# Performance work log

Measured on AMD Instinct MI355X. Metric: run time of the kernel, lower is better.

The kernel has to match this reference:

```python
import jax, jax.numpy as jnp
import numpy as np

H = 4        # nhead
TEMP = 0.1   # temperature
TOP_K = 5
SHAPE_EPS = 1e-5


def _ln(x, g, b):
    m = x.mean(-1, keepdims=True)
    v = ((x - m) ** 2).mean(-1, keepdims=True)
    return (x - m) / jnp.sqrt(v + SHAPE_EPS) * g + b


def _mha(x, Wqkv, bqkv, Wo, bo):
    B, L, D = x.shape
    Dh = D // H
    qkv = x @ Wqkv.T + bqkv                     # [B,L,3D]
    q, k, v = jnp.split(qkv, 3, axis=-1)
    q = q.reshape(B, L, H, Dh)
    k = k.reshape(B, L, H, Dh)
    v = v.reshape(B, L, H, Dh)
    att = jnp.einsum('bqhd,bkhd->bhqk', q, k) * (1.0 / np.sqrt(Dh))
    att = jax.nn.softmax(att, axis=-1)
    o = jnp.einsum('bhqk,bkhd->bqhd', att, v).reshape(B, L, D)
    return o @ Wo.T + bo


def _pattern_encoder(x, cls_token, Wqkv, bqkv, Wo, bo, ln1_g, ln1_b,
                     W1, b1, W2, b2, ln2_g, ln2_b, proj_W, proj_b, proj_g, proj_bb):
    B, L, D = x.shape
    h = jnp.concatenate([jnp.broadcast_to(cls_token, (B, 1, D)), x], axis=1)  # [B,L+1,D]
    for i in range(Wqkv.shape[0]):  # num_layers=2, post-norm (PyTorch default)
        a = _mha(h, Wqkv[i], bqkv[i], Wo[i], bo[i])
        h = _ln(h + a, ln1_g[i], ln1_b[i])
        f = jax.nn.gelu(h @ W1[i].T + b1[i], approximate=False) @ W2[i].T + b2[i]
        h = _ln(h + f, ln2_g[i], ln2_b[i])
    cls_out = h[:, 0, :]
    return _ln(cls_out @ proj_W.T + proj_b, proj_g, proj_bb)  # [B,d_repr]


def _value_encoder(xm, vW1, vb1, v_g, v_b, vW2, vb2):
    hh = _ln(xm @ vW1.T + vb1, v_g, v_b)
    return jax.nn.gelu(hh, approximate=False) @ vW2.T + vb2


def setup_inputs() -> dict:
    B, L, D, DR, N, P, NL = 64, 512, 512, 128, 10000, 96, 2
    key = jax.random.key(0)
    ks = jax.random.split(key, 16)
    sc = 0.02
    inp = {
        'query': jax.random.normal(ks[0], (B, L, D), jnp.float32),
        'memory_keys': jax.random.normal(ks[1], (N, DR), jnp.float32),
        'memory_values': jax.random.normal(ks[2], (N, P, D), jnp.float32),
        'cls_token': jax.random.normal(ks[3], (1, 1, D), jnp.float32) * sc,
        'Wqkv': jax.random.normal(ks[4], (NL, 3 * D, D), jnp.float32) * sc,
        'bqkv': jnp.zeros((NL, 3 * D), jnp.float32),
        'Wo': jax.random.normal(ks[5], (NL, D, D), jnp.float32) * sc,
        'bo': jnp.zeros((NL, D), jnp.float32),
        'ln1_g': jnp.ones((NL, D), jnp.float32),
        'ln1_b': jnp.zeros((NL, D), jnp.float32),
        'W1': jax.random.normal(ks[6], (NL, 2 * D, D), jnp.float32) * sc,
        'b1': jnp.zeros((NL, 2 * D), jnp.float32),
        'W2': jax.random.normal(ks[7], (NL, D, 2 * D), jnp.float32) * sc,
        'b2': jnp.zeros((NL, D), jnp.float32),
        'ln2_g': jnp.ones((NL, D), jnp.float32),
        'ln2_b': jnp.zeros((NL, D), jnp.float32),
        'proj_W': jax.random.normal(ks[8], (DR, D), jnp.float32) * sc,
        'proj_b': jnp.zeros((DR,), jnp.float32),
        'proj_g': jnp.ones((DR,), jnp.float32),
        'proj_bb': jnp.zeros((DR,), jnp.float32),
        'vW1': jax.random.normal(ks[9], (DR, D), jnp.float32) * sc,
        'vb1': jnp.zeros((DR,), jnp.float32),
        'v_g': jnp.ones((DR,), jnp.float32),
        'v_b': jnp.zeros((DR,), jnp.float32),
        'vW2': jax.random.normal(ks[10], (DR, DR), jnp.float32) * sc,
        'vb2': jnp.zeros((DR,), jnp.float32),
        'shape_w': jnp.float32(0.5),
    }
    return inp


def reference(query, memory_keys, memory_values, cls_token, Wqkv, bqkv, Wo, bo,
              ln1_g, ln1_b, W1, b1, W2, b2, ln2_g, ln2_b,
              proj_W, proj_b, proj_g, proj_bb, vW1, vb1, v_g, v_b, vW2, vb2, shape_w):
    q_repr = _pattern_encoder(query, cls_token, Wqkv, bqkv, Wo, bo, ln1_g, ln1_b,
                              W1, b1, W2, b2, ln2_g, ln2_b, proj_W, proj_b, proj_g, proj_bb)
    q_val = _value_encoder(query.mean(axis=1), vW1, vb1, v_g, v_b, vW2, vb2)
    qk = shape_w * q_repr + (1.0 - shape_w) * q_val              # [B,DR]
    # squared euclidean distance, expanded form (same math as sum((a-b)^2))
    d = ((qk ** 2).sum(-1)[:, None]
         - 2.0 * qk @ memory_keys.T
         + (memory_keys ** 2).sum(-1)[None, :])                  # [B,N]
    sim = -d / TEMP
    top_scores, top_idx = jax.lax.top_k(sim, TOP_K)              # [B,K]
    weights = jax.nn.softmax(top_scores, axis=-1)
    retrieved = memory_values[top_idx]                           # [B,K,P,D]
    return retrieved, weights
```

## Files before the change

kernel.cpp:

```cpp
#include <hip/hip_runtime.h>
#include <math.h>

#define B_    64
#define LQ    512
#define LC    513
#define DD    512
#define HH    4
#define DH    128
#define DRr   128
#define NKEYS 10000
#define PP    96
#define TOPK  5
#define MROWS (B_*LC)
#define VTSTRIDE 544

typedef __attribute__((ext_vector_type(8))) short short8v;
typedef __attribute__((ext_vector_type(4))) float f32x4;
typedef __attribute__((ext_vector_type(16))) float f32x16;

static __device__ __forceinline__ float gelu_exact(float x) {
    return 0.5f * x * (1.0f + erff(x * 0.70710678118654752440f));
}

static __device__ __forceinline__ unsigned short f2bf(float x) {
    union { float f; unsigned u; } v; v.f = x;
    unsigned r = v.u + 0x7fff + ((v.u >> 16) & 1);
    return (unsigned short)(r >> 16);
}
static __device__ __forceinline__ float bf2f(unsigned short h) {
    union { float f; unsigned u; } v; v.u = ((unsigned)h) << 16;
    return v.f;
}
static __device__ __forceinline__ void split_bf(float x, unsigned short& hi, unsigned short& lo) {
    hi = f2bf(x);
    lo = f2bf(x - bf2f(hi));
}

static __device__ __forceinline__ int xcd_swz(int orig, int nwg) {
    int xcd = orig & 7;
    int lid = orig >> 3;
    int q = nwg >> 3, r = nwg & 7;
    int base = (xcd < r) ? xcd * (q + 1) : r * (q + 1) + (xcd - r) * q;
    return base + lid;
}

static __device__ __forceinline__ void gload16(const unsigned short* g, unsigned short* l) {
    __builtin_amdgcn_global_load_lds(
        (const __attribute__((address_space(1))) unsigned*)g,
        (__attribute__((address_space(3))) unsigned*)l, 16, 0, 0);
}

__global__ __launch_bounds__(256)
void split_kernel(const float* __restrict__ x, unsigned short* __restrict__ hi,
                  unsigned short* __restrict__ lo, int n4)
{
    int i = blockIdx.x * blockDim.x + threadIdx.x;
    if (i >= n4) return;
    float4 v = ((const float4*)x)[i];
    unsigned short h0,h1,h2,h3,l0,l1,l2,l3;
    split_bf(v.x,h0,l0); split_bf(v.y,h1,l1); split_bf(v.z,h2,l2); split_bf(v.w,h3,l3);
    ((uint2*)hi)[i] = make_uint2((unsigned)h0 | ((unsigned)h1 << 16), (unsigned)h2 | ((unsigned)h3 << 16));
    ((uint2*)lo)[i] = make_uint2((unsigned)l0 | ((unsigned)l1 << 16), (unsigned)l2 | ((unsigned)l3 << 16));
}

__global__ __launch_bounds__(128)
void concat_cls(const float* __restrict__ query, const float* __restrict__ cls,
                float* __restrict__ h, unsigned short* __restrict__ h_hi,
                unsigned short* __restrict__ h_lo)
{
    int row = blockIdx.x;
    int t = threadIdx.x;
    int b = row / LC, r = row - b * LC;
    const float* src = (r == 0) ? cls : (query + ((size_t)b * LQ + (r - 1)) * DD);
    float4 v = *(const float4*)(src + t * 4);
    *(float4*)(h + (size_t)row * DD + t * 4) = v;
    unsigned short hs[4], ls[4];
    split_bf(v.x, hs[0], ls[0]); split_bf(v.y, hs[1], ls[1]);
    split_bf(v.z, hs[2], ls[2]); split_bf(v.w, hs[3], ls[3]);
    size_t o = (size_t)row * DD + t * 4;
    ((uint2*)(h_hi))[o >> 2] = make_uint2((unsigned)hs[0] | ((unsigned)hs[1]<<16),
                                          (unsigned)hs[2] | ((unsigned)hs[3]<<16));
    ((uint2*)(h_lo))[o >> 2] = make_uint2((unsigned)ls[0] | ((unsigned)ls[1]<<16),
                                          (unsigned)ls[2] | ((unsigned)ls[3]<<16));
}

#define BM 128
#define BN 128
#define BK 32

#define MFMA32(a, b, c) __builtin_amdgcn_mfma_f32_32x32x16_bf16(a, b, c, 0, 0, 0)

template<int MODE>
__global__ __launch_bounds__(256)
void gemm3(const unsigned short* __restrict__ Ahi, const unsigned short* __restrict__ Alo,
           const unsigned short* __restrict__ Whi, const unsigned short* __restrict__ Wlo,
           const float* __restrict__ bias, const float* __restrict__ res,
           float* __restrict__ Cf, unsigned short* __restrict__ Chi,
           unsigned short* __restrict__ Clo, unsigned* __restrict__ Vix,
           int M, int N, int K, int NBN)
{
    __shared__ __align__(16) unsigned short POOL[16384];
    unsigned short* LAh = POOL;
    unsigned short* LAl = POOL + 4096;
    unsigned short* LBh = POOL + 8192;
    unsigned short* LBl = POOL + 12288;

    const int t = threadIdx.x;
    const int lane = t & 63, w = t >> 6;
    const int wr = w >> 1, wc = w & 1;
    const int wg = xcd_swz(blockIdx.x, gridDim.x);
    const int bm = wg / NBN, bn = wg - bm * NBN;
    const int row0 = bm * BM, col0 = bn * BN;

    const int srow = t >> 2;
    const int sg   = t & 3;
    const int glog = sg ^ (srow & 3);
    int ar0 = row0 + srow;      if (ar0 >= M) ar0 = M - 1;
    int ar1 = row0 + srow + 64; if (ar1 >= M) ar1 = M - 1;
    const size_t aoff0 = (size_t)ar0 * K + glog * 8;
    const size_t aoff1 = (size_t)ar1 * K + glog * 8;
    const size_t boff0 = (size_t)(col0 + srow) * K + glog * 8;
    const size_t boff1 = (size_t)(col0 + srow + 64) * K + glog * 8;
    const int ldso0 = t * 8;
    const int ldso1 = t * 8 + 2048;

    f32x16 acc[2][2];
    #pragma unroll
    for (int m = 0; m < 2; m++)
        #pragma unroll
        for (int n = 0; n < 2; n++)
            #pragma unroll
            for (int i = 0; i < 16; i++) acc[m][n][i] = 0.f;

    const int cl = lane & 31;
    const int kg = lane >> 5;
    const int cl3 = cl & 3;

    const int KT = K / BK;
    for (int kt = 0; kt < KT; kt++) {
        const int k0 = kt * BK;
        __syncthreads();
        gload16(Ahi + aoff0 + k0, &LAh[ldso0]);
        gload16(Ahi + aoff1 + k0, &LAh[ldso1]);
        gload16(Alo + aoff0 + k0, &LAl[ldso0]);
        gload16(Alo + aoff1 + k0, &LAl[ldso1]);
        gload16(Whi + boff0 + k0, &LBh[ldso0]);
        gload16(Whi + boff1 + k0, &LBh[ldso1]);
        gload16(Wlo + boff0 + k0, &LBl[ldso0]);
        gload16(Wlo + boff1 + k0, &LBl[ldso1]);
        __syncthreads();

        #pragma unroll
        for (int ks = 0; ks < 2; ks++) {
            const int blkswz = ((ks * 2 + kg) ^ cl3) * 8;
            short8v ah[2], al[2], bh[2], bl[2];
            #pragma unroll
            for (int m = 0; m < 2; m++) {
                int off = (wr * 64 + m * 32 + cl) * 32 + blkswz;
                ah[m] = *(const short8v*)&LAh[off];
                al[m] = *(const short8v*)&LAl[off];
            }
            #pragma unroll
            for (int n = 0; n < 2; n++) {
                int off = (wc * 64 + n * 32 + cl) * 32 + blkswz;
                bh[n] = *(const short8v*)&LBh[off];
                bl[n] = *(const short8v*)&LBl[off];
            }
            #pragma unroll
            for (int m = 0; m < 2; m++)
                #pragma unroll
                for (int n = 0; n < 2; n++) {
                    acc[m][n] = MFMA32(ah[m], bh[n], acc[m][n]);
                    acc[m][n] = MFMA32(al[m], bh[n], acc[m][n]);
                    acc[m][n] = MFMA32(ah[m], bl[n], acc[m][n]);
                }
        }
    }

    if (MODE == 3 && col0 >= 1024) {
        const int hh = (col0 - 1024) >> 7;
        unsigned* VS = (unsigned*)POOL;
        const int bb0 = row0 / LC;
        const int bound = (bb0 + 1) * LC;
        const int ddl = t >> 3, j0 = (t & 7) * 16;
        #pragma unroll
        for (int p = 0; p < 4; p++) {
            __syncthreads();
            if (wc == (p >> 1)) {
                const int ccl = col0 + wc * 64 + (p & 1) * 32 + cl;
                const float bcol = bias[ccl];
                #pragma unroll
                for (int m = 0; m < 2; m++) {
                    const int lrb = wr * 64 + m * 32 + 4 * kg;
                    #pragma unroll
                    for (int q = 0; q < 4; q++)
                        #pragma unroll
                        for (int r = 0; r < 4; r++) {
                            float v = ((p & 1) ? acc[m][1][q * 4 + r]
                                               : acc[m][0][q * 4 + r]) + bcol;
                            unsigned short hv, lv;
                            split_bf(v, hv, lv);
                            VS[cl * 129 + lrb + 8 * q + r] =
                                (unsigned)hv | ((unsigned)lv << 16);
                        }
                }
            }
            __syncthreads();
            long long vb0 = (long long)((bb0 * HH + hh) * DH + p * 32 + ddl) * VTSTRIDE
                            - (long long)bb0 * LC;
            long long vb1 = (long long)(((bb0 + 1) * HH + hh) * DH + p * 32 + ddl) * VTSTRIDE
                            - (long long)(bb0 + 1) * LC;
            #pragma unroll
            for (int j = 0; j < 16; j++) {
                int row = row0 + j0 + j;
                if (row < M) {
                    long long vi = (row < bound ? vb0 : vb1) + row;
                    Vix[vi] = VS[ddl * 129 + j0 + j];
                }
            }
        }
        return;
    }

    #pragma unroll
    for (int m = 0; m < 2; m++) {
        const int rb = row0 + wr * 64 + m * 32 + 4 * kg;
        #pragma unroll
        for (int n = 0; n < 2; n++) {
            const int cc = col0 + wc * 64 + n * 32 + cl;
            const float bcol = bias[cc];
            #pragma unroll
            for (int q = 0; q < 4; q++) {
                #pragma unroll
                for (int r = 0; r < 4; r++) {
                    int row = rb + 8 * q + r;
                    if (row < M) {
                        float v = acc[m][n][q * 4 + r] + bcol;
                        if (MODE == 1) v += res[(size_t)row * N + cc];
                        if (MODE == 2) {
                            v = gelu_exact(v);
                            unsigned short hv, lv;
                            split_bf(v, hv, lv);
                            Chi[(size_t)row * N + cc] = hv;
                            Clo[(size_t)row * N + cc] = lv;
                        } else if (MODE == 3) {
                            unsigned short hv, lv;
                            split_bf(v, hv, lv);
                            Chi[(size_t)row * 1024 + cc] = hv;
                            Clo[(size_t)row * 1024 + cc] = lv;
                        } else {
                            Cf[(size_t)row * N + cc] = v;
                        }
                    }
                }
            }
        }
    }
}

#define AQT 64
#define AKT 32
#define NKT2 17
#define MFMA16(a, b, c) __builtin_amdgcn_mfma_f32_16x16x32_bf16(a, b, c, 0, 0, 0)
__global__ __launch_bounds__(256)
void attn_mfma(const unsigned short* __restrict__ qkhi, const unsigned short* __restrict__ qklo,
               const unsigned* __restrict__ vtx,
               unsigned short* __restrict__ ohi, unsigned short* __restrict__ olo)
{
    __shared__ __align__(16) unsigned short SM[24064];
    #define KH(r,d) SM[(r)*136 + (d)]
    #define KL(r,d) SM[4352 + (r)*136 + (d)]
    #define VH(d,k) SM[8704 + (d)*40 + (k)]
    #define VL(d,k) SM[13824 + (d)*40 + (k)]
    #define PH(r,k) SM[18944 + (r)*40 + (k)]
    #define PL(r,k) SM[21504 + (r)*40 + (k)]
    #define OS(r,d) SM[(r)*136 + (d)]

    const int t = threadIdx.x;
    const int lane = t & 63, w = t >> 6;
    const int id = xcd_swz(blockIdx.x, gridDim.x);
    const int qt = id % 9;
    const int hb = id / 9;
    const int h = hb & 3, b = hb >> 2;
    const int q0 = qt * AQT;
    const int c = lane & 15, g = lane >> 4;
    const float SCALE = 0.08838834764831845f;

    short8v qh[4], ql[4];
    {
        int qrow = b * LC + q0 + w * 16 + c;
        if (qrow > MROWS - 1) qrow = MROWS - 1;
        const unsigned short* bh_ = qkhi + (size_t)qrow * 1024 + h * DH;
        const unsigned short* bl_ = qklo + (size_t)qrow * 1024 + h * DH;
        #pragma unroll
        for (int ks = 0; ks < 4; ks++) {
            qh[ks] = *(const short8v*)(bh_ + ks * 32 + g * 8);
            ql[ks] = *(const short8v*)(bl_ + ks * 32 + g * 8);
        }
    }

    float m_r[4], l_r[4];
    #pragma unroll
    for (int r = 0; r < 4; r++) { m_r[r] = -INFINITY; l_r[r] = 0.f; }
    f32x4 acc_o[8];
    #pragma unroll
    for (int n = 0; n < 8; n++) { acc_o[n][0]=0.f; acc_o[n][1]=0.f; acc_o[n][2]=0.f; acc_o[n][3]=0.f; }

    const int skr = t >> 3, skd = (t & 7) * 16;
    const int svd = t >> 1, svk = (t & 1) * 16;

    for (int kt = 0; kt < NKT2; kt++) {
        __syncthreads();
        {
            int krow = b * LC + kt * AKT + skr;
            if (krow > MROWS - 1) krow = MROWS - 1;
            const unsigned short* kb  = qkhi + (size_t)krow * 1024 + 512 + h * DH + skd;
            const unsigned short* kbl = qklo + (size_t)krow * 1024 + 512 + h * DH + skd;
            *(short8v*)&KH(skr, skd)     = *(const short8v*)kb;
            *(short8v*)&KH(skr, skd + 8) = *(const short8v*)(kb + 8);
            *(short8v*)&KL(skr, skd)     = *(const short8v*)kbl;
            *(short8v*)&KL(skr, skd + 8) = *(const short8v*)(kbl + 8);
            const unsigned* vb = vtx + ((size_t)((b * HH + h) * DH + svd)) * VTSTRIDE + kt * AKT + svk;
            uint4 a0 = *(const uint4*)(vb);
            uint4 a1 = *(const uint4*)(vb + 4);
            uint4 a2 = *(const uint4*)(vb + 8);
            uint4 a3 = *(const uint4*)(vb + 12);
            uint4 hA, hB, lA, lB;
            hA.x = (a0.x & 0xffffu) | (a0.y << 16);
            hA.y = (a0.z & 0xffffu) | (a0.w << 16);
            hA.z = (a1.x & 0xffffu) | (a1.y << 16);
            hA.w = (a1.z & 0xffffu) | (a1.w << 16);
            hB.x = (a2.x & 0xffffu) | (a2.y << 16);
            hB.y = (a2.z & 0xffffu) | (a2.w << 16);
            hB.z = (a3.x & 0xffffu) | (a3.y << 16);
            hB.w = (a3.z & 0xffffu) | (a3.w << 16);
            lA.x = (a0.x >> 16) | (a0.y & 0xffff0000u);
            lA.y = (a0.z >> 16) | (a0.w & 0xffff0000u);
            lA.z = (a1.x >> 16) | (a1.y & 0xffff0000u);
            lA.w = (a1.z >> 16) | (a1.w & 0xffff0000u);
            lB.x = (a2.x >> 16) | (a2.y & 0xffff0000u);
            lB.y = (a2.z >> 16) | (a2.w & 0xffff0000u);
            lB.z = (a3.x >> 16) | (a3.y & 0xffff0000u);
            lB.w = (a3.z >> 16) | (a3.w & 0xffff0000u);
            *(uint4*)&VH(svd, svk)     = hA;
            *(uint4*)&VH(svd, svk + 8) = hB;
            *(uint4*)&VL(svd, svk)     = lA;
            *(uint4*)&VL(svd, svk + 8) = lB;
        }
        __syncthreads();

        f32x4 s[2];
        s[0][0]=s[0][1]=s[0][2]=s[0][3]=0.f;
        s[1][0]=s[1][1]=s[1][2]=s[1][3]=0.f;
        #pragma unroll
        for (int n = 0; n < 2; n++) {
            #pragma unroll
            for (int ks = 0; ks < 4; ks++) {
                short8v kh = *(const short8v*)&KH(n * 16 + c, ks * 32 + g * 8);
                short8v kl = *(const short8v*)&KL(n * 16 + c, ks * 32 + g * 8);
                s[n] = MFMA16(qh[ks], kh, s[n]);
                s[n] = MFMA16(ql[ks], kh, s[n]);
                s[n] = MFMA16(qh[ks], kl, s[n]);
            }
        }

        #pragma unroll
        for (int n = 0; n < 2; n++) {
            bool oob = (kt * 32 + n * 16 + c) >= LC;
            #pragma unroll
            for (int r = 0; r < 4; r++) {
                float sv = s[n][r] * SCALE;
                s[n][r] = oob ? -INFINITY : sv;
            }
        }

        float alpha[4], p0v[4], p1v[4];
        #pragma unroll
        for (int r = 0; r < 4; r++) {
            float rm = fmaxf(s[0][r], s[1][r]);
            #pragma unroll
            for (int off = 1; off < 16; off <<= 1) rm = fmaxf(rm, __shfl_xor(rm, off));
            float mn = fmaxf(m_r[r], rm);
            float p0 = expf(s[0][r] - mn);
            float p1 = expf(s[1][r] - mn);
            float ts = p0 + p1;
            #pragma unroll
            for (int off = 1; off < 16; off <<= 1) ts += __shfl_xor(ts, off);
            float al = expf(m_r[r] - mn);
            m_r[r] = mn;
            l_r[r] = al * l_r[r] + ts;
            alpha[r] = al;
            p0v[r] = p0; p1v[r] = p1;
        }

        #pragma unroll
        for (int n = 0; n < 8; n++)
            #pragma unroll
            for (int r = 0; r < 4; r++) acc_o[n][r] *= alpha[r];

        #pragma unroll
        for (int r = 0; r < 4; r++) {
            unsigned short ph, pl;
            split_bf(p0v[r], ph, pl);
            PH(w * 16 + g * 4 + r, c) = ph;
            PL(w * 16 + g * 4 + r, c) = pl;
            split_bf(p1v[r], ph, pl);
            PH(w * 16 + g * 4 + r, 16 + c) = ph;
            PL(w * 16 + g * 4 + r, 16 + c) = pl;
        }
        __syncthreads();

        short8v pah = *(const short8v*)&PH(w * 16 + c, g * 8);
        short8v pal = *(const short8v*)&PL(w * 16 + c, g * 8);
        #pragma unroll
        for (int n = 0; n < 8; n++) {
            short8v vh = *(const short8v*)&VH(n * 16 + c, g * 8);
            short8v vl = *(const short8v*)&VL(n * 16 + c, g * 8);
            acc_o[n] = MFMA16(pah, vh, acc_o[n]);
            acc_o[n] = MFMA16(pal, vh, acc_o[n]);
            acc_o[n] = MFMA16(pah, vl, acc_o[n]);
        }
    }

    float inv[4];
    #pragma unroll
    for (int r = 0; r < 4; r++) inv[r] = 1.0f / l_r[r];

    const int orow = t >> 2, oc0 = (t & 3) * 32;
    #pragma unroll
    for (int pass = 0; pass < 2; pass++) {
        __syncthreads();
        #pragma unroll
        for (int n = 0; n < 8; n++)
            #pragma unroll
            for (int r = 0; r < 4; r++) {
                float v = acc_o[n][r] * inv[r];
                unsigned short hv, lv;
                split_bf(v, hv, lv);
                OS(w * 16 + g * 4 + r, n * 16 + c) = pass ? lv : hv;
            }
        __syncthreads();
        int grow = q0 + orow;
        if (grow < LC) {
            unsigned short* dst = (pass ? olo : ohi) + ((size_t)(b * LC + grow)) * DD + h * DH + oc0;
            #pragma unroll
            for (int u = 0; u < 4; u++)
                *(short8v*)(dst + u * 8) = *(const short8v*)&OS(orow, oc0 + u * 8);
        }
    }
    #undef KH
    #undef KL
    #undef VH
    #undef VL
    #undef PH
    #undef PL
    #undef OS
}

__global__ __launch_bounds__(128)
void ln512(const float* __restrict__ X, const float* __restrict__ g,
           const float* __restrict__ bb, float* __restrict__ Y,
           unsigned short* __restrict__ Yhi, unsigned short* __restrict__ Ylo)
{
    __shared__ float red[2];
    int row = blockIdx.x, t = threadIdx.x;
    const float* x = X + (size_t)row * DD;
    float4 v = *(const float4*)(x + t * 4);
    float s = v.x + v.y + v.z + v.w;
    #pragma unroll
    for (int off = 1; off < 64; off <<= 1) s += __shfl_xor(s, off);
    if ((t & 63) == 0) red[t >> 6] = s;
    __syncthreads();
    float mean = (red[0] + red[1]) * (1.0f / 512.0f);
    __syncthreads();
    float d0 = v.x - mean, d1 = v.y - mean, d2 = v.z - mean, d3 = v.w - mean;
    float s2 = d0 * d0 + d1 * d1 + d2 * d2 + d3 * d3;
    #pragma unroll
    for (int off = 1; off < 64; off <<= 1) s2 += __shfl_xor(s2, off);
    if ((t & 63) == 0) red[t >> 6] = s2;
    __syncthreads();
    float var = (red[0] + red[1]) * (1.0f / 512.0f);
    float rstd = 1.0f / sqrtf(var + 1e-5f);
    float4 gv = *(const float4*)(g + t * 4);
    float4 bv = *(const float4*)(bb + t * 4);
    float4 ov;
    ov.x = d0 * rstd * gv.x + bv.x;
    ov.y = d1 * rstd * gv.y + bv.y;
    ov.z = d2 * rstd * gv.z + bv.z;
    ov.w = d3 * rstd * gv.w + bv.w;
    size_t o = (size_t)row * DD + t * 4;
    *(float4*)(Y + o) = ov;
    unsigned short hs[4], ls[4];
    split_bf(ov.x, hs[0], ls[0]); split_bf(ov.y, hs[1], ls[1]);
    split_bf(ov.z, hs[2], ls[2]); split_bf(ov.w, hs[3], ls[3]);
    ((uint2*)Yhi)[o >> 2] = make_uint2((unsigned)hs[0] | ((unsigned)hs[1]<<16),
                                       (unsigned)hs[2] | ((unsigned)hs[3]<<16));
    ((uint2*)Ylo)[o >> 2] = make_uint2((unsigned)ls[0] | ((unsigned)ls[1]<<16),
                                       (unsigned)ls[2] | ((unsigned)ls[3]<<16));
}

__global__ __launch_bounds__(128)
void mean_part(const float* __restrict__ query, float* __restrict__ part)
{
    int b = blockIdx.x, ch = blockIdx.y, t = threadIdx.x;
    const float* base = query + ((size_t)b * LQ + ch * 64) * DD + t * 4;
    float ax = 0.f, ay = 0.f, az = 0.f, aw = 0.f;
    for (int l = 0; l < 64; l++) {
        float4 v = *(const float4*)(base + (size_t)l * DD);
        ax += v.x; ay += v.y; az += v.z; aw += v.w;
    }
    *(float4*)(part + ((size_t)(b * 8 + ch)) * DD + t * 4) = make_float4(ax, ay, az, aw);
}

__global__ __launch_bounds__(128)
void mean_fin(const float* __restrict__ part, float* __restrict__ xm)
{
    int b = blockIdx.x, t = threadIdx.x;
    float ax = 0.f, ay = 0.f, az = 0.f, aw = 0.f;
    #pragma unroll
    for (int ch = 0; ch < 8; ch++) {
        float4 v = *(const float4*)(part + ((size_t)(b * 8 + ch)) * DD + t * 4);
        ax += v.x; ay += v.y; az += v.z; aw += v.w;
    }
    *(float4*)(xm + (size_t)b * DD + t * 4) =
        make_float4(ax * (1.f/512.f), ay * (1.f/512.f), az * (1.f/512.f), aw * (1.f/512.f));
}

static __device__ __forceinline__ float block128_sum(float x, float* red, int t) {
    #pragma unroll
    for (int off = 1; off < 64; off <<= 1) x += __shfl_xor(x, off);
    if ((t & 63) == 0) red[t >> 6] = x;
    __syncthreads();
    float r = red[0] + red[1];
    __syncthreads();
    return r;
}

__global__ __launch_bounds__(128)
void proj_ln(const float* __restrict__ h, const float* __restrict__ pW, const float* __restrict__ pb,
             const float* __restrict__ pg, const float* __restrict__ pbb, float* __restrict__ q_repr)
{
    __shared__ float xs[DD];
    __shared__ float red[2];
    int b = blockIdx.x, t = threadIdx.x;
    *(float4*)&xs[t * 4] = *(const float4*)(h + (size_t)(b * LC) * DD + t * 4);
    __syncthreads();
    const float* w = pW + (size_t)t * DD;
    float acc = pb[t];
    for (int k = 0; k < DD; k += 4) {
        float4 a = *(const float4*)&xs[k];
        float4 ww = *(const float4*)(w + k);
        acc += a.x * ww.x + a.y * ww.y + a.z * ww.z + a.w * ww.w;
    }
    float mean = block128_sum(acc, red, t) * (1.f / 128.f);
    float dx = acc - mean;
    float var = block128_sum(dx * dx, red, t) * (1.f / 128.f);
    float rstd = 1.0f / sqrtf(var + 1e-5f);
    q_repr[(size_t)b * DRr + t] = dx * rstd * pg[t] + pbb[t];
}

__global__ __launch_bounds__(128)
void venc(const float* __restrict__ xm, const float* __restrict__ vW1, const float* __restrict__ vb1,
          const float* __restrict__ vg, const float* __restrict__ vb,
          const float* __restrict__ vW2, const float* __restrict__ vb2,
          float* __restrict__ q_val)
{
    __shared__ float xs[DD];
    __shared__ float hg[DRr];
    __shared__ float red[2];
    int b = blockIdx.x, t = threadIdx.x;
    *(float4*)&xs[t * 4] = *(const float4*)(xm + (size_t)b * DD + t * 4);
    __syncthreads();
    const float* w = vW1 + (size_t)t * DD;
    float acc = vb1[t];
    for (int k = 0; k < DD; k += 4) {
        float4 a = *(const float4*)&xs[k];
        float4 ww = *(const float4*)(w + k);
        acc += a.x * ww.x + a.y * ww.y + a.z * ww.z + a.w * ww.w;
    }
    float mean = block128_sum(acc, red, t) * (1.f / 128.f);
    float dx = acc - mean;
    float var = block128_sum(dx * dx, red, t) * (1.f / 128.f);
    float rstd = 1.0f / sqrtf(var + 1e-5f);
    float hn = dx * rstd * vg[t] + vb[t];
    hg[t] = gelu_exact(hn);
    __syncthreads();
    const float* w2 = vW2 + (size_t)t * DRr;
    float acc2 = vb2[t];
    for (int k = 0; k < DRr; k += 4) {
        float4 a = *(const float4*)&hg[k];
        float4 ww = *(const float4*)(w2 + k);
        acc2 += a.x * ww.x + a.y * ww.y + a.z * ww.z + a.w * ww.w;
    }
    q_val[(size_t)b * DRr + t] = acc2;
}

__global__ void combine_qk(const float* __restrict__ qr, const float* __restrict__ qv,
                           const float* __restrict__ swp, float* __restrict__ qk)
{
    int i = blockIdx.x * blockDim.x + threadIdx.x;
    if (i < B_ * DRr) {
        float sw = swp[0];
        qk[i] = sw * qr[i] + (1.f - sw) * qv[i];
    }
}

#define SIMCH 10
__global__ __launch_bounds__(256)
void sim_kernel(const float* __restrict__ qk, const float* __restrict__ mkeys, float* __restrict__ sim)
{
    __shared__ float qs[DRr];
    int b = blockIdx.x, ch = blockIdx.y, t = threadIdx.x;
    if (t < DRr) qs[t] = qk[(size_t)b * DRr + t];
    __syncthreads();
    float qn = 0.f;
    #pragma unroll 8
    for (int i = 0; i < DRr; i++) qn += qs[i] * qs[i];
    int n0 = ch * (NKEYS / SIMCH), n1 = n0 + (NKEYS / SIMCH);
    for (int n = n0 + t; n < n1; n += 256) {
        const float* kr = mkeys + (size_t)n * DRr;
        float dot = 0.f, kn = 0.f;
        #pragma unroll 8
        for (int i = 0; i < DRr; i += 4) {
            float4 kv = *(const float4*)(kr + i);
            dot += qs[i] * kv.x + qs[i + 1] * kv.y + qs[i + 2] * kv.z + qs[i + 3] * kv.w;
            kn  += kv.x * kv.x + kv.y * kv.y + kv.z * kv.z + kv.w * kv.w;
        }
        float d = qn - 2.f * dot + kn;
        sim[(size_t)b * NKEYS + n] = -d / 0.1f;
    }
}

static __device__ __forceinline__ void topk_insert(float* v, int* id, float x, int n) {
    bool better = (x > v[TOPK - 1]) || (x == v[TOPK - 1] && n < id[TOPK - 1]);
    if (better) {
        v[TOPK - 1] = x; id[TOPK - 1] = n;
        #pragma unroll
        for (int k = TOPK - 1; k > 0; k--) {
            bool sw = (v[k] > v[k - 1]) || (v[k] == v[k - 1] && id[k] < id[k - 1]);
            if (!sw) break;
            float tv = v[k]; v[k] = v[k - 1]; v[k - 1] = tv;
            int ti = id[k]; id[k] = id[k - 1]; id[k - 1] = ti;
        }
    }
}

__global__ __launch_bounds__(256)
void topk_kernel(const float* __restrict__ sim, int* __restrict__ topidx, float* __restrict__ wout)
{
    __shared__ float sv[256][TOPK];
    __shared__ int   si[256][TOPK];
    int b = blockIdx.x, t = threadIdx.x;
    float v[TOPK]; int id[TOPK];
    #pragma unroll
    for (int k = 0; k < TOPK; k++) { v[k] = -INFINITY; id[k] = 0x7fffffff; }
    for (int n = t; n < NKEYS; n += 256) {
        topk_insert(v, id, sim[(size_t)b * NKEYS + n], n);
    }
    #pragma unroll
    for (int k = 0; k < TOPK; k++) { sv[t][k] = v[k]; si[t][k] = id[k]; }
    for (int strd = 128; strd >= 1; strd >>= 1) {
        __syncthreads();
        if (t < strd) {
            #pragma unroll
            for (int k = 0; k < TOPK; k++) topk_insert(v, id, sv[t + strd][k], si[t + strd][k]);
            #pragma unroll
            for (int k = 0; k < TOPK; k++) { sv[t][k] = v[k]; si[t][k] = id[k]; }
        }
    }
    if (t == 0) {
        float m = v[0];
        float e[TOPK]; float sum = 0.f;
        #pragma unroll
        for (int k = 0; k < TOPK; k++) { e[k] = expf(v[k] - m); sum += e[k]; }
        #pragma unroll
        for (int k = 0; k < TOPK; k++) {
            wout[(size_t)b * TOPK + k] = e[k] / sum;
            topidx[b * TOPK + k] = id[k];
        }
    }
}

__global__ __launch_bounds__(128)
void gather_kernel(const float* __restrict__ mv, const int* __restrict__ topidx, float* __restrict__ out)
{
    int blk = blockIdx.x;
    int b = blk / (TOPK * PP);
    int rem = blk - b * (TOPK * PP);
    int k = rem / PP;
    int p = rem - k * PP;
    int idx = topidx[b * TOPK + k];
    const float4* src = (const float4*)(mv + ((size_t)idx * PP + p) * DD);
    float4* dst = (float4*)(out + (size_t)blk * DD);
    dst[threadIdx.x] = src[threadIdx.x];
}

extern "C" void kernel_launch(void* const* d_in, const int* in_sizes, int n_in,
                              void* d_out, int out_size, void* d_ws, size_t ws_size,
                              hipStream_t stream) {
    const float* query = (const float*)d_in[0];
    const float* mkeys = (const float*)d_in[1];
    const float* mvals = (const float*)d_in[2];
    const float* cls   = (const float*)d_in[3];
    const float* Wqkv  = (const float*)d_in[4];
    const float* bqkv  = (const float*)d_in[5];
    const float* Wo    = (const float*)d_in[6];
    const float* bo    = (const float*)d_in[7];
    const float* ln1g  = (const float*)d_in[8];
    const float* ln1b  = (const float*)d_in[9];
    const float* W1    = (const float*)d_in[10];
    const float* b1    = (const float*)d_in[11];
    const float* W2    = (const float*)d_in[12];
    const float* b2    = (const float*)d_in[13];
    const float* ln2g  = (const float*)d_in[14];
    const float* ln2b  = (const float*)d_in[15];
    const float* pW    = (const float*)d_in[16];
    const float* pb    = (const float*)d_in[17];
    const float* pg    = (const float*)d_in[18];
    const float* pbb   = (const float*)d_in[19];
    const float* vW1   = (const float*)d_in[20];
    const float* vb1   = (const float*)d_in[21];
    const float* vg    = (const float*)d_in[22];
    const float* vb    = (const float*)d_in[23];
    const float* vW2   = (const float*)d_in[24];
    const float* vb2   = (const float*)d_in[25];
    const float* swp   = (const float*)d_in[26];
    float* out = (float*)d_out;

    float* ws    = (float*)d_ws;
    float* h     = ws;
    float* preln = h + (size_t)MROWS * DD;
    unsigned short* h_hi  = (unsigned short*)(preln + (size_t)MROWS * DD);
    unsigned short* h_lo  = h_hi  + (size_t)MROWS * DD;
    unsigned short* mid_hi = h_lo + (size_t)MROWS * DD;
    unsigned short* mid_lo = mid_hi + (size_t)MROWS * 1024;
    unsigned short* qkhi  = mid_lo + (size_t)MROWS * 1024;
    unsigned short* qklo  = qkhi  + (size_t)MROWS * 1024;
    unsigned* vtx         = (unsigned*)(qklo + (size_t)MROWS * 1024);
    unsigned short* wq_hi = (unsigned short*)(vtx + (size_t)32768 * VTSTRIDE);
    unsigned short* wq_lo = wq_hi + (size_t)2 * 1536 * DD;
    unsigned short* wo_hi = wq_lo + (size_t)2 * 1536 * DD;
    unsigned short* wo_lo = wo_hi + (size_t)2 * DD * DD;
    unsigned short* w1_hi = wo_lo + (size_t)2 * DD * DD;
    unsigned short* w1_lo = w1_hi + (size_t)2 * 1024 * DD;
    unsigned short* w2_hi = w1_lo + (size_t)2 * 1024 * DD;
    unsigned short* w2_lo = w2_hi + (size_t)2 * DD * 1024;
    float* xm   = (float*)(w2_lo + (size_t)2 * DD * 1024);
    float* qval = xm   + (size_t)B_ * DD;
    float* qrep = qval + (size_t)B_ * DRr;
    float* qkc  = qrep + (size_t)B_ * DRr;
    float* simb = qkc  + (size_t)B_ * DRr;
    int*   tidx = (int*)(simb + (size_t)B_ * NKEYS);
    float* mpart = (float*)(tidx + 512);
    (void)ws_size; (void)in_sizes; (void)n_in; (void)out_size;

    {
        int n4;
        n4 = 2 * 1536 * DD / 4;
        split_kernel<<<(n4 + 255) / 256, 256, 0, stream>>>(Wqkv, wq_hi, wq_lo, n4);
        n4 = 2 * DD * DD / 4;
        split_kernel<<<(n4 + 255) / 256, 256, 0, stream>>>(Wo, wo_hi, wo_lo, n4);
        n4 = 2 * 1024 * DD / 4;
        split_kernel<<<(n4 + 255) / 256, 256, 0, stream>>>(W1, w1_hi, w1_lo, n4);
        n4 = 2 * DD * 1024 / 4;
        split_kernel<<<(n4 + 255) / 256, 256, 0, stream>>>(W2, w2_hi, w2_lo, n4);
    }

    concat_cls<<<MROWS, 128, 0, stream>>>(query, cls, h, h_hi, h_lo);

    for (int l = 0; l < 2; l++) {
        const unsigned short* wqh = wq_hi + (size_t)l * 1536 * DD;
        const unsigned short* wql = wq_lo + (size_t)l * 1536 * DD;
        const unsigned short* woh = wo_hi + (size_t)l * DD * DD;
        const unsigned short* wol = wo_lo + (size_t)l * DD * DD;
        const unsigned short* w1h = w1_hi + (size_t)l * 1024 * DD;
        const unsigned short* w1l = w1_lo + (size_t)l * 1024 * DD;
        const unsigned short* w2h = w2_hi + (size_t)l * DD * 1024;
        const unsigned short* w2l = w2_lo + (size_t)l * DD * 1024;
        const float* bq  = bqkv + (size_t)l * 1536;
        const float* bol = bo   + (size_t)l * DD;
        const float* g1  = ln1g + (size_t)l * DD;
        const float* be1 = ln1b + (size_t)l * DD;
        const float* b1l = b1   + (size_t)l * 1024;
        const float* b2l = b2   + (size_t)l * DD;
        const float* g2  = ln2g + (size_t)l * DD;
        const float* be2 = ln2b + (size_t)l * DD;

        gemm3<3><<<257 * 12, 256, 0, stream>>>(h_hi, h_lo, wqh, wql, bq, nullptr,
                                               nullptr, qkhi, qklo, vtx,
                                               MROWS, 1536, DD, 12);
        attn_mfma<<<9 * HH * B_, 256, 0, stream>>>(qkhi, qklo, vtx, h_hi, h_lo);
        gemm3<1><<<257 * 4, 256, 0, stream>>>(h_hi, h_lo, woh, wol, bol, h,
                                              preln, nullptr, nullptr, nullptr,
                                              MROWS, DD, DD, 4);
        ln512<<<MROWS, 128, 0, stream>>>(preln, g1, be1, h, h_hi, h_lo);
        gemm3<2><<<257 * 8, 256, 0, stream>>>(h_hi, h_lo, w1h, w1l, b1l, nullptr,
                                              nullptr, mid_hi, mid_lo, nullptr,
                                              MROWS, 1024, DD, 8);
        gemm3<1><<<257 * 4, 256, 0, stream>>>(mid_hi, mid_lo, w2h, w2l, b2l, h,
                                              preln, nullptr, nullptr, nullptr,
                                              MROWS, DD, 1024, 4);
        ln512<<<MROWS, 128, 0, stream>>>(preln, g2, be2, h, h_hi, h_lo);
    }

    proj_ln<<<B_, 128, 0, stream>>>(h, pW, pb, pg, pbb, qrep);
    mean_part<<<dim3(B_, 8), 128, 0, stream>>>(query, mpart);
    mean_fin<<<B_, 128, 0, stream>>>(mpart, xm);
    venc<<<B_, 128, 0, stream>>>(xm, vW1, vb1, vg, vb, vW2, vb2, qval);
    combine_qk<<<(B_ * DRr + 255) / 256, 256, 0, stream>>>(qrep, qval, swp, qkc);
    sim_kernel<<<dim3(B_, SIMCH), 256, 0, stream>>>(qkc, mkeys, simb);
    topk_kernel<<<B_, 256, 0, stream>>>(simb, tidx, out + (size_t)B_ * TOPK * PP * DD);
    gather_kernel<<<B_ * TOPK * PP, 128, 0, stream>>>(mvals, tidx, out);
}
```

Baseline: 2.415 ms.

## Double-buffer GEMM LDS tiles, prefetch attention K/V, one-row-per-wave LN/concat

The split-bf16 GEMM now double-buffers its LDS tiles and issues the next k-tile's async global-to-LDS loads before computing the current one, replacing two __syncthreads per step with waitcnt plus barrier. The attention kernel prefetches the next K/V tile into registers during compute, drops one barrier and raises wave priority around the MFMA blocks. LayerNorm and the concat kernel map one row per 64-lane wave with 4 rows per block, which removes shared-memory reductions and block syncs. Doubling GEMM LDS to 64KB may cut occupancy, and the hand-placed waitcnt and barriers are easy to get wrong.

```diff
diff --git a/kernel.cpp b/kernel.cpp
--- a/kernel.cpp
+++ b/kernel.cpp
@@ -63,25 +63,36 @@
     ((uint2*)lo)[i] = make_uint2((unsigned)l0 | ((unsigned)l1 << 16), (unsigned)l2 | ((unsigned)l3 << 16));
 }
 
-__global__ __launch_bounds__(128)
+__global__ __launch_bounds__(256)
 void concat_cls(const float* __restrict__ query, const float* __restrict__ cls,
                 float* __restrict__ h, unsigned short* __restrict__ h_hi,
                 unsigned short* __restrict__ h_lo)
 {
-    int row = blockIdx.x;
-    int t = threadIdx.x;
+    int row = blockIdx.x * 4 + (threadIdx.x >> 6);
+    int lane = threadIdx.x & 63;
     int b = row / LC, r = row - b * LC;
-    const float* src = (r == 0) ? cls : (query + ((size_t)b * LQ + (r - 1)) * DD);
-    float4 v = *(const float4*)(src + t * 4);
-    *(float4*)(h + (size_t)row * DD + t * 4) = v;
-    unsigned short hs[4], ls[4];
-    split_bf(v.x, hs[0], ls[0]); split_bf(v.y, hs[1], ls[1]);
-    split_bf(v.z, hs[2], ls[2]); split_bf(v.w, hs[3], ls[3]);
-    size_t o = (size_t)row * DD + t * 4;
-    ((uint2*)(h_hi))[o >> 2] = make_uint2((unsigned)hs[0] | ((unsigned)hs[1]<<16),
-                                          (unsigned)hs[2] | ((unsigned)hs[3]<<16));
-    ((uint2*)(h_lo))[o >> 2] = make_uint2((unsigned)ls[0] | ((unsigned)ls[1]<<16),
-                                          (unsigned)ls[2] | ((unsigned)ls[3]<<16));
+    const float* src = (r == 0) ? (cls + lane * 8)
+                                : (query + ((size_t)b * LQ + (r - 1)) * DD + lane * 8);
+    float4 v0 = *(const float4*)src;
+    float4 v1 = *(const float4*)(src + 4);
+    size_t o = (size_t)row * DD + lane * 8;
+    *(float4*)(h + o) = v0;
+    *(float4*)(h + o + 4) = v1;
+    float vv[8] = {v0.x,v0.y,v0.z,v0.w,v1.x,v1.y,v1.z,v1.w};
+    unsigned short hs[8], ls[8];
+    #pragma unroll
+    for (int i = 0; i < 8; i++) split_bf(vv[i], hs[i], ls[i]);
+    uint4 hv, lv;
+    hv.x = (unsigned)hs[0] | ((unsigned)hs[1] << 16);
+    hv.y = (unsigned)hs[2] | ((unsigned)hs[3] << 16);
+    hv.z = (unsigned)hs[4] | ((unsigned)hs[5] << 16);
+    hv.w = (unsigned)hs[6] | ((unsigned)hs[7] << 16);
+    lv.x = (unsigned)ls[0] | ((unsigned)ls[1] << 16);
+    lv.y = (unsigned)ls[2] | ((unsigned)ls[3] << 16);
+    lv.z = (unsigned)ls[4] | ((unsigned)ls[5] << 16);
+    lv.w = (unsigned)ls[6] | ((unsigned)ls[7] << 16);
+    *(uint4*)(h_hi + o) = hv;
+    *(uint4*)(h_lo + o) = lv;
 }
 
 #define BM 128
@@ -99,11 +110,7 @@
            unsigned short* __restrict__ Clo, unsigned* __restrict__ Vix,
            int M, int N, int K, int NBN)
 {
-    __shared__ __align__(16) unsigned short POOL[16384];
-    unsigned short* LAh = POOL;
-    unsigned short* LAl = POOL + 4096;
-    unsigned short* LBh = POOL + 8192;
-    unsigned short* LBl = POOL + 12288;
+    __shared__ __align__(16) unsigned short POOL[32768];
 
     const int t = threadIdx.x;
     const int lane = t & 63, w = t >> 6;
@@ -137,18 +144,34 @@
     const int cl3 = cl & 3;
 
     const int KT = K / BK;
+    gload16(Ahi + aoff0, &POOL[ldso0]);
+    gload16(Ahi + aoff1, &POOL[ldso1]);
+    gload16(Alo + aoff0, &POOL[4096 + ldso0]);
+    gload16(Alo + aoff1, &POOL[4096 + ldso1]);
+    gload16(Whi + boff0, &POOL[8192 + ldso0]);
+    gload16(Whi + boff1, &POOL[8192 + ldso1]);
+    gload16(Wlo + boff0, &POOL[12288 + ldso0]);
+    gload16(Wlo + boff1, &POOL[12288 + ldso1]);
+
     for (int kt = 0; kt < KT; kt++) {
-        const int k0 = kt * BK;
-        __syncthreads();
-        gload16(Ahi + aoff0 + k0, &LAh[ldso0]);
-        gload16(Ahi + aoff1 + k0, &LAh[ldso1]);
-        gload16(Alo + aoff0 + k0, &LAl[ldso0]);
-        gload16(Alo + aoff1 + k0, &LAl[ldso1]);
-        gload16(Whi + boff0 + k0, &LBh[ldso0]);
-        gload16(Whi + boff1 + k0, &LBh[ldso1]);
-        gload16(Wlo + boff0 + k0, &LBl[ldso0]);
-        gload16(Wlo + boff1 + k0, &LBl[ldso1]);
-        __syncthreads();
+        const int cb = (kt & 1) * 16384;
+        const int nb = 16384 - cb;
+        if (kt + 1 < KT) {
+            const int k0n = (kt + 1) * BK;
+            gload16(Ahi + aoff0 + k0n, &POOL[nb + ldso0]);
+            gload16(Ahi + aoff1 + k0n, &POOL[nb + ldso1]);
+            gload16(Alo + aoff0 + k0n, &POOL[nb + 4096 + ldso0]);
+            gload16(Alo + aoff1 + k0n, &POOL[nb + 4096 + ldso1]);
+            gload16(Whi + boff0 + k0n, &POOL[nb + 8192 + ldso0]);
+            gload16(Whi + boff1 + k0n, &POOL[nb + 8192 + ldso1]);
+            gload16(Wlo + boff0 + k0n, &POOL[nb + 12288 + ldso0]);
+            gload16(Wlo + boff1 + k0n, &POOL[nb + 12288 + ldso1]);
+            asm volatile("s_waitcnt vmcnt(8)" ::: "memory");
+        } else {
+            asm volatile("s_waitcnt vmcnt(0)" ::: "memory");
+        }
+        __builtin_amdgcn_s_barrier();
+        __builtin_amdgcn_sched_barrier(0);
 
         #pragma unroll
         for (int ks = 0; ks < 2; ks++) {
@@ -156,15 +179,15 @@
             short8v ah[2], al[2], bh[2], bl[2];
             #pragma unroll
             for (int m = 0; m < 2; m++) {
-                int off = (wr * 64 + m * 32 + cl) * 32 + blkswz;
-                ah[m] = *(const short8v*)&LAh[off];
-                al[m] = *(const short8v*)&LAl[off];
+                int off = cb + (wr * 64 + m * 32 + cl) * 32 + blkswz;
+                ah[m] = *(const short8v*)&POOL[off];
+                al[m] = *(const short8v*)&POOL[off + 4096];
             }
             #pragma unroll
             for (int n = 0; n < 2; n++) {
-                int off = (wc * 64 + n * 32 + cl) * 32 + blkswz;
-                bh[n] = *(const short8v*)&LBh[off];
-                bl[n] = *(const short8v*)&LBl[off];
+                int off = cb + (wc * 64 + n * 32 + cl) * 32 + blkswz;
+                bh[n] = *(const short8v*)&POOL[off + 8192];
+                bl[n] = *(const short8v*)&POOL[off + 12288];
             }
             #pragma unroll
             for (int m = 0; m < 2; m++)
@@ -175,6 +198,7 @@
                     acc[m][n] = MFMA32(ah[m], bl[n], acc[m][n]);
                 }
         }
+        __builtin_amdgcn_s_barrier();
     }
 
     if (MODE == 3 && col0 >= 1024) {
@@ -308,50 +332,74 @@
 
     const int skr = t >> 3, skd = (t & 7) * 16;
     const int svd = t >> 1, svk = (t & 1) * 16;
+    const unsigned short* kbase  = qkhi + 512 + h * DH + skd;
+    const unsigned short* kbasel = qklo + 512 + h * DH + skd;
+    const unsigned* vbase = vtx + ((size_t)((b * HH + h) * DH + svd)) * VTSTRIDE + svk;
+
+    short8v rk0, rk1, rl0, rl1;
+    uint4 rv0, rv1, rv2, rv3;
+    {
+        int krow = b * LC + skr; if (krow > MROWS - 1) krow = MROWS - 1;
+        const unsigned short* kb  = kbase  + (size_t)krow * 1024;
+        const unsigned short* kbl = kbasel + (size_t)krow * 1024;
+        rk0 = *(const short8v*)kb;  rk1 = *(const short8v*)(kb + 8);
+        rl0 = *(const short8v*)kbl; rl1 = *(const short8v*)(kbl + 8);
+        rv0 = *(const uint4*)(vbase);
+        rv1 = *(const uint4*)(vbase + 4);
+        rv2 = *(const uint4*)(vbase + 8);
+        rv3 = *(const uint4*)(vbase + 12);
+    }
 
     for (int kt = 0; kt < NKT2; kt++) {
-        __syncthreads();
+        __builtin_amdgcn_s_barrier();
+        *(short8v*)&KH(skr, skd)     = rk0;
+        *(short8v*)&KH(skr, skd + 8) = rk1;
+        *(short8v*)&KL(skr, skd)     = rl0;
+        *(short8v*)&KL(skr, skd + 8) = rl1;
         {
-            int krow = b * LC + kt * AKT + skr;
-            if (krow > MROWS - 1) krow = MROWS - 1;
-            const unsigned short* kb  = qkhi + (size_t)krow * 1024 + 512 + h * DH + skd;
-            const unsigned short* kbl = qklo + (size_t)krow * 1024 + 512 + h * DH + skd;
-            *(short8v*)&KH(skr, skd)     = *(const short8v*)kb;
-            *(short8v*)&KH(skr, skd + 8) = *(const short8v*)(kb + 8);
-            *(short8v*)&KL(skr, skd)     = *(const short8v*)kbl;
-            *(short8v*)&KL(skr, skd + 8) = *(const short8v*)(kbl + 8);
-            const unsigned* vb = vtx + ((size_t)((b * HH + h) * DH + svd)) * VTSTRIDE + kt * AKT + svk;
-            uint4 a0 = *(const uint4*)(vb);
-            uint4 a1 = *(const uint4*)(vb + 4);
-            uint4 a2 = *(const uint4*)(vb + 8);
-            uint4 a3 = *(const uint4*)(vb + 12);
             uint4 hA, hB, lA, lB;
-            hA.x = (a0.x & 0xffffu) | (a0.y << 16);
-            hA.y = (a0.z & 0xffffu) | (a0.w << 16);
-            hA.z = (a1.x & 0xffffu) | (a1.y << 16);
-            hA.w = (a1.z & 0xffffu) | (a1.w << 16);
-            hB.x = (a2.x & 0xffffu) | (a2.y << 16);
-            hB.y = (a2.z & 0xffffu) | (a2.w << 16);
-            hB.z = (a3.x & 0xffffu) | (a3.y << 16);
-            hB.w = (a3.z & 0xffffu) | (a3.w << 16);
-            lA.x = (a0.x >> 16) | (a0.y & 0xffff0000u);
-            lA.y = (a0.z >> 16) | (a0.w & 0xffff0000u);
-            lA.z = (a1.x >> 16) | (a1.y & 0xffff0000u);
-            lA.w = (a1.z >> 16) | (a1.w & 0xffff0000u);
-            lB.x = (a2.x >> 16) | (a2.y & 0xffff0000u);
-            lB.y = (a2.z >> 16) | (a2.w & 0xffff0000u);
-            lB.z = (a3.x >> 16) | (a3.y & 0xffff0000u);
-            lB.w = (a3.z >> 16) | (a3.w & 0xffff0000u);
+            hA.x = (rv0.x & 0xffffu) | (rv0.y << 16);
+            hA.y = (rv0.z & 0xffffu) | (rv0.w << 16);
+            hA.z = (rv1.x & 0xffffu) | (rv1.y << 16);
+            hA.w = (rv1.z & 0xffffu) | (rv1.w << 16);
+            hB.x = (rv2.x & 0xffffu) | (rv2.y << 16);
+            hB.y = (rv2.z & 0xffffu) | (rv2.w << 16);
+            hB.z = (rv3.x & 0xffffu) | (rv3.y << 16);
+            hB.w = (rv3.z & 0xffffu) | (rv3.w << 16);
+            lA.x = (rv0.x >> 16) | (rv0.y & 0xffff0000u);
+            lA.y = (rv0.z >> 16) | (rv0.w & 0xffff0000u);
+            lA.z = (rv1.x >> 16) | (rv1.y & 0xffff0000u);
+            lA.w = (rv1.z >> 16) | (rv1.w & 0xffff0000u);
+            lB.x = (rv2.x >> 16) | (rv2.y & 0xffff0000u);
+            lB.y = (rv2.z >> 16) | (rv2.w & 0xffff0000u);
+            lB.z = (rv3.x >> 16) | (rv3.y & 0xffff0000u);
+            lB.w = (rv3.z >> 16) | (rv3.w & 0xffff0000u);
             *(uint4*)&VH(svd, svk)     = hA;
             *(uint4*)&VH(svd, svk + 8) = hB;
             *(uint4*)&VL(svd, svk)     = lA;
             *(uint4*)&VL(svd, svk + 8) = lB;
         }
-        __syncthreads();
+        if (kt + 1 < NKT2) {
+            int krow = b * LC + (kt + 1) * AKT + skr;
+            if (krow > MROWS - 1) krow = MROWS - 1;
+            const unsigned short* kb  = kbase  + (size_t)krow * 1024;
+            const unsigned short* kbl = kbasel + (size_t)krow * 1024;
+            rk0 = *(const short8v*)kb;  rk1 = *(const short8v*)(kb + 8);
+            rl0 = *(const short8v*)kbl; rl1 = *(const short8v*)(kbl + 8);
+            const unsigned* vb = vbase + (kt + 1) * AKT;
+            rv0 = *(const uint4*)(vb);
+            rv1 = *(const uint4*)(vb + 4);
+            rv2 = *(const uint4*)(vb + 8);
+            rv3 = *(const uint4*)(vb + 12);
+        }
+        asm volatile("s_waitcnt lgkmcnt(0)" ::: "memory");
+        __builtin_amdgcn_s_barrier();
+        __builtin_amdgcn_sched_barrier(0);
 
         f32x4 s[2];
         s[0][0]=s[0][1]=s[0][2]=s[0][3]=0.f;
         s[1][0]=s[1][1]=s[1][2]=s[1][3]=0.f;
+        __builtin_amdgcn_s_setprio(1);
         #pragma unroll
         for (int n = 0; n < 2; n++) {
             #pragma unroll
@@ -363,6 +411,7 @@
                 s[n] = MFMA16(qh[ks], kl, s[n]);
             }
         }
+        __builtin_amdgcn_s_setprio(0);
 
         #pragma unroll
         for (int n = 0; n < 2; n++) {
@@ -408,10 +457,9 @@
             PH(w * 16 + g * 4 + r, 16 + c) = ph;
             PL(w * 16 + g * 4 + r, 16 + c) = pl;
         }
-        __syncthreads();
-
         short8v pah = *(const short8v*)&PH(w * 16 + c, g * 8);
         short8v pal = *(const short8v*)&PL(w * 16 + c, g * 8);
+        __builtin_amdgcn_s_setprio(1);
         #pragma unroll
         for (int n = 0; n < 8; n++) {
             short8v vh = *(const short8v*)&VH(n * 16 + c, g * 8);
@@ -420,6 +468,7 @@
             acc_o[n] = MFMA16(pal, vh, acc_o[n]);
             acc_o[n] = MFMA16(pah, vl, acc_o[n]);
         }
+        __builtin_amdgcn_s_setprio(0);
     }
 
     float inv[4];
@@ -457,46 +506,57 @@
     #undef OS
 }
 
-__global__ __launch_bounds__(128)
+__global__ __launch_bounds__(256)
 void ln512(const float* __restrict__ X, const float* __restrict__ g,
            const float* __restrict__ bb, float* __restrict__ Y,
            unsigned short* __restrict__ Yhi, unsigned short* __restrict__ Ylo)
 {
-    __shared__ float red[2];
-    int row = blockIdx.x, t = threadIdx.x;
-    const float* x = X + (size_t)row * DD;
-    float4 v = *(const float4*)(x + t * 4);
-    float s = v.x + v.y + v.z + v.w;
+    int row = blockIdx.x * 4 + (threadIdx.x >> 6);
+    int lane = threadIdx.x & 63;
+    const float* x = X + (size_t)row * DD + lane * 8;
+    float4 v0 = *(const float4*)x;
+    float4 v1 = *(const float4*)(x + 4);
+    float vv[8] = {v0.x,v0.y,v0.z,v0.w,v1.x,v1.y,v1.z,v1.w};
+    float s = 0.f;
+    #pragma unroll
+    for (int i = 0; i < 8; i++) s += vv[i];
     #pragma unroll
     for (int off = 1; off < 64; off <<= 1) s += __shfl_xor(s, off);
-    if ((t & 63) == 0) red[t >> 6] = s;
-    __syncthreads();
-    float mean = (red[0] + red[1]) * (1.0f / 512.0f);
-    __syncthreads();
-    float d0 = v.x - mean, d1 = v.y - mean, d2 = v.z - mean, d3 = v.w - mean;
-    float s2 = d0 * d0 + d1 * d1 + d2 * d2 + d3 * d3;
+    float mean = s * (1.0f / 512.0f);
+    float d[8], s2 = 0.f;
+    #pragma unroll
+    for (int i = 0; i < 8; i++) { d[i] = vv[i] - mean; s2 += d[i] * d[i]; }
     #pragma unroll
     for (int off = 1; off < 64; off <<= 1) s2 += __shfl_xor(s2, off);
-    if ((t & 63) == 0) red[t >> 6] = s2;
-    __syncthreads();
-    float var = (red[0] + red[1]) * (1.0f / 512.0f);
+    float var = s2 * (1.0f / 512.0f);
     float rstd = 1.0f / sqrtf(var + 1e-5f);
-    float4 gv = *(const float4*)(g + t * 4);
-    float4 bv = *(const float4*)(bb + t * 4);
-    float4 ov;
-    ov.x = d0 * rstd * gv.x + bv.x;
-    ov.y = d1 * rstd * gv.y + bv.y;
-    ov.z = d2 * rstd * gv.z + bv.z;
-    ov.w = d3 * rstd * gv.w + bv.w;
-    size_t o = (size_t)row * DD + t * 4;
-    *(float4*)(Y + o) = ov;
-    unsigned short hs[4], ls[4];
-    split_bf(ov.x, hs[0], ls[0]); split_bf(ov.y, hs[1], ls[1]);
-    split_bf(ov.z, hs[2], ls[2]); split_bf(ov.w, hs[3], ls[3]);
-    ((uint2*)Yhi)[o >> 2] = make_uint2((unsigned)hs[0] | ((unsigned)hs[1]<<16),
-                                       (unsigned)hs[2] | ((unsigned)hs[3]<<16));
-    ((uint2*)Ylo)[o >> 2] = make_uint2((unsigned)ls[0] | ((unsigned)ls[1]<<16),
-                                       (unsigned)ls[2] | ((unsigned)ls[3]<<16));
+    float4 g0 = *(const float4*)(g + lane * 8);
+    float4 g1 = *(const float4*)(g + lane * 8 + 4);
+    float4 b0 = *(const float4*)(bb + lane * 8);
+    float4 b1 = *(const float4*)(bb + lane * 8 + 4);
+    float gg[8] = {g0.x,g0.y,g0.z,g0.w,g1.x,g1.y,g1.z,g1.w};
+    float bv[8] = {b0.x,b0.y,b0.z,b0.w,b1.x,b1.y,b1.z,b1.w};
+    float ov[8];
+    unsigned short hs[8], ls[8];
+    #pragma unroll
+    for (int i = 0; i < 8; i++) {
+        ov[i] = d[i] * rstd * gg[i] + bv[i];
+        split_bf(ov[i], hs[i], ls[i]);
+    }
+    size_t o = (size_t)row * DD + lane * 8;
+    *(float4*)(Y + o)     = make_float4(ov[0], ov[1], ov[2], ov[3]);
+    *(float4*)(Y + o + 4) = make_float4(ov[4], ov[5], ov[6], ov[7]);
+    uint4 hv, lv;
+    hv.x = (unsigned)hs[0] | ((unsigned)hs[1] << 16);
+    hv.y = (unsigned)hs[2] | ((unsigned)hs[3] << 16);
+    hv.z = (unsigned)hs[4] | ((unsigned)hs[5] << 16);
+    hv.w = (unsigned)hs[6] | ((unsigned)hs[7] << 16);
+    lv.x = (unsigned)ls[0] | ((unsigned)ls[1] << 16);
+    lv.y = (unsigned)ls[2] | ((unsigned)ls[3] << 16);
+    lv.z = (unsigned)ls[4] | ((unsigned)ls[5] << 16);
+    lv.w = (unsigned)ls[6] | ((unsigned)ls[7] << 16);
+    *(uint4*)(Yhi + o) = hv;
+    *(uint4*)(Ylo + o) = lv;
 }
 
 __global__ __launch_bounds__(128)
@@ -766,7 +826,7 @@
         split_kernel<<<(n4 + 255) / 256, 256, 0, stream>>>(W2, w2_hi, w2_lo, n4);
     }
 
-    concat_cls<<<MROWS, 128, 0, stream>>>(query, cls, h, h_hi, h_lo);
+    concat_cls<<<MROWS / 4, 256, 0, stream>>>(query, cls, h, h_hi, h_lo);
 
     for (int l = 0; l < 2; l++) {
         const unsigned short* wqh = wq_hi + (size_t)l * 1536 * DD;
@@ -793,14 +853,14 @@
         gemm3<1><<<257 * 4, 256, 0, stream>>>(h_hi, h_lo, woh, wol, bol, h,
                                               preln, nullptr, nullptr, nullptr,
                                               MROWS, DD, DD, 4);
-        ln512<<<MROWS, 128, 0, stream>>>(preln, g1, be1, h, h_hi, h_lo);
+        ln512<<<MROWS / 4, 256, 0, stream>>>(preln, g1, be1, h, h_hi, h_lo);
         gemm3<2><<<257 * 8, 256, 0, stream>>>(h_hi, h_lo, w1h, w1l, b1l, nullptr,
                                               nullptr, mid_hi, mid_lo, nullptr,
                                               MROWS, 1024, DD, 8);
         gemm3<1><<<257 * 4, 256, 0, stream>>>(mid_hi, mid_lo, w2h, w2l, b2l, h,
                                               preln, nullptr, nullptr, nullptr,
                                               MROWS, DD, 1024, 4);
-        ln512<<<MROWS, 128, 0, stream>>>(preln, g2, be2, h, h_hi, h_lo);
+        ln512<<<MROWS / 4, 256, 0, stream>>>(preln, g2, be2, h, h_hi, h_lo);
     }
 
     proj_ln<<<B_, 128, 0, stream>>>(h, pW, pb, pg, pbb, qrep);
```

New measurement: 2.490 ms. +3.1%, slower.
